# Performance work log

Hardware: AMD Instinct MI355X
Metric: run time of the kernel (lower is better)

## Reference

```python
import jax, jax.numpy as jnp
import numpy as np

N = 50000        # nodes (== input_dim, featureless layer)
E = 400000       # edges in sparse support
HID = 200        # hidden dim hardcoded in GCN
NUM_CLASSES = 10


def setup_inputs() -> dict:
    key = jax.random.key(0)
    k1, k2, k3, k4 = jax.random.split(key, 4)
    return {
        "x": jnp.zeros((N, 1), dtype=jnp.float32),  # unused (featureless layer1)
        "support_rows": jax.random.randint(k1, (E,), 0, N, dtype=jnp.int32),
        "support_cols": jax.random.randint(k2, (E,), 0, N, dtype=jnp.int32),
        "support_vals": jax.random.uniform(k3, (E,), dtype=jnp.float32),
        "W0": jax.random.normal(k4, (N, HID), dtype=jnp.float32),
        "W2": jax.random.normal(jax.random.fold_in(key, 5), (HID, NUM_CLASSES), dtype=jnp.float32),
    }


def reference(x, support_rows, support_cols, support_vals, W0, W2):
    # Layer 1 (featureless): pre_sup = W0; out = A @ W0 via sparse edge list.
    # SpMM as gather + scale + segment-sum:
    gathered = W0[support_cols] * support_vals[:, None]          # [E, HID]
    h = jax.ops.segment_sum(gathered, support_rows, num_segments=N)  # [N, HID]
    h = jax.nn.relu(h)
    # Layer 2 (SimpleGraphConvolution, no act, no bias): h @ W2
    return h @ W2                                                # [N, NUM_CLASSES]
```

## Files before the change

kernel.cpp:

```cpp
#include <hip/hip_runtime.h>

#define N_NODES 50000
#define N_EDGES 400000
#define HID     200
#define NCLS    10
#define SLOTS   40


__device__ __forceinline__ unsigned bf16rn(float f) {
    unsigned u = __float_as_uint(f);
    return (u + 0x7FFFu + ((u >> 16) & 1u)) >> 16;
}
__device__ __forceinline__ float bl(unsigned u) { return __uint_as_float(u << 16); }
__device__ __forceinline__ float bh(unsigned u) { return __uint_as_float(u & 0xFFFF0000u); }

__global__ __launch_bounds__(256) void k_convert(const float4* __restrict__ W04,
                                                 uint4* __restrict__ W0h4,
                                                 int4* __restrict__ cnt4) {
    int i = blockIdx.x * 256 + threadIdx.x;
    if (i < 12504) cnt4[i] = make_int4(0, 0, 0, 0);
    if (i >= (N_NODES * HID) / 8) return;
    float4 f0 = W04[i * 2];
    float4 f1 = W04[i * 2 + 1];
    uint4 o;
    o.x = bf16rn(f0.x) | (bf16rn(f0.y) << 16);
    o.y = bf16rn(f0.z) | (bf16rn(f0.w) << 16);
    o.z = bf16rn(f1.x) | (bf16rn(f1.y) << 16);
    o.w = bf16rn(f1.z) | (bf16rn(f1.w) << 16);
    W0h4[i] = o;
}

__global__ void k_place(const int* __restrict__ rows, const int* __restrict__ cols,
                        const float* __restrict__ vals,
                        int* __restrict__ cnt, unsigned* __restrict__ ev) {
    int e = blockIdx.x * 256 + threadIdx.x;
    if (e >= N_EDGES) return;
    int r = rows[e];
    int pos = atomicAdd(&cnt[r], 1);
    if (pos < SLOTS)
        ev[(size_t)r * SLOTS + pos] = (bf16rn(vals[e]) << 16) | (unsigned)cols[e];
}

__global__ __launch_bounds__(256, 4) void gcn_fused(
        const int*      __restrict__ cnt,
        const unsigned* __restrict__ ev,
        const ushort*   __restrict__ W0h,
        const float*    __restrict__ W2,
        float*          __restrict__ out) {
    __shared__ float w2p[25 * 81 + 7];
    {
        int t = threadIdx.x;
        if (t < HID) {
            float* dst = &w2p[(t >> 3) * 81 + (t & 7) * 10];
            const float* src = &W2[t * NCLS];
            *reinterpret_cast<float4*>(dst)     = *reinterpret_cast<const float4*>(src);
            *reinterpret_cast<float4*>(dst + 4) = *reinterpret_cast<const float4*>(src + 4);
            *reinterpret_cast<float2*>(dst + 8) = *reinterpret_cast<const float2*>(src + 8);
        }
    }
    __syncthreads();

    const int lane = threadIdx.x & 63;
    const int hl   = lane & 31;
    const bool selB = lane >= 32;
    const int lp   = min(hl, 24);
    const int off8 = lp * 8;
    const float* __restrict__ w2l = &w2p[lp * 81];

    const int w  = (blockIdx.x * 256 + threadIdx.x) >> 6;
    const int wu = __builtin_amdgcn_readfirstlane(w);

    const int4 cc = *reinterpret_cast<const int4*>(cnt + 4 * wu);
    const int nA = min(cc.x, SLOTS), nB = min(cc.y, SLOTS);
    const int nC = min(cc.z, SLOTS), nD = min(cc.w, SLOTS);
    const int n0 = selB ? nC : nA;
    const int n1 = selB ? nD : nB;
    const int ntm = (max(max(nA, nB), max(nC, nD)) + 7) >> 3;

    const unsigned* __restrict__ evp = ev + (size_t)(4 * wu) * SLOTS;

    float hk0[8] = {0.f, 0.f, 0.f, 0.f, 0.f, 0.f, 0.f, 0.f};
    float hk1[8] = {0.f, 0.f, 0.f, 0.f, 0.f, 0.f, 0.f, 0.f};

    for (int t = 0; t < ntm; ++t) {
        const int s = t * 8;
        const uint4 a0 = *reinterpret_cast<const uint4*>(evp + s);
        const uint4 a1 = *reinterpret_cast<const uint4*>(evp + s + 4);
        const uint4 b0 = *reinterpret_cast<const uint4*>(evp + SLOTS + s);
        const uint4 b1 = *reinterpret_cast<const uint4*>(evp + SLOTS + s + 4);
        const uint4 c0 = *reinterpret_cast<const uint4*>(evp + 2 * SLOTS + s);
        const uint4 c1 = *reinterpret_cast<const uint4*>(evp + 2 * SLOTS + s + 4);
        const uint4 d0 = *reinterpret_cast<const uint4*>(evp + 3 * SLOTS + s);
        const uint4 d1 = *reinterpret_cast<const uint4*>(evp + 3 * SLOTS + s + 4);

        unsigned u0 = (s + 0 < n0) ? (selB ? c0.x : a0.x) : 0u;
        unsigned u1 = (s + 1 < n0) ? (selB ? c0.y : a0.y) : 0u;
        unsigned u2 = (s + 2 < n0) ? (selB ? c0.z : a0.z) : 0u;
        unsigned u3 = (s + 3 < n0) ? (selB ? c0.w : a0.w) : 0u;
        unsigned u4 = (s + 4 < n0) ? (selB ? c1.x : a1.x) : 0u;
        unsigned u5 = (s + 5 < n0) ? (selB ? c1.y : a1.y) : 0u;
        unsigned u6 = (s + 6 < n0) ? (selB ? c1.z : a1.z) : 0u;
        unsigned u7 = (s + 7 < n0) ? (selB ? c1.w : a1.w) : 0u;
        unsigned v0 = (s + 0 < n1) ? (selB ? d0.x : b0.x) : 0u;
        unsigned v1 = (s + 1 < n1) ? (selB ? d0.y : b0.y) : 0u;
        unsigned v2 = (s + 2 < n1) ? (selB ? d0.z : b0.z) : 0u;
        unsigned v3 = (s + 3 < n1) ? (selB ? d0.w : b0.w) : 0u;
        unsigned v4 = (s + 4 < n1) ? (selB ? d1.x : b1.x) : 0u;
        unsigned v5 = (s + 5 < n1) ? (selB ? d1.y : b1.y) : 0u;
        unsigned v6 = (s + 6 < n1) ? (selB ? d1.z : b1.z) : 0u;
        unsigned v7 = (s + 7 < n1) ? (selB ? d1.w : b1.w) : 0u;

        uint4 gA0 = *reinterpret_cast<const uint4*>(W0h + (size_t)(u0 & 0xFFFFu) * HID + off8);
        uint4 gA1 = *reinterpret_cast<const uint4*>(W0h + (size_t)(u1 & 0xFFFFu) * HID + off8);
        uint4 gA2 = *reinterpret_cast<const uint4*>(W0h + (size_t)(u2 & 0xFFFFu) * HID + off8);
        uint4 gA3 = *reinterpret_cast<const uint4*>(W0h + (size_t)(u3 & 0xFFFFu) * HID + off8);
        uint4 gA4 = *reinterpret_cast<const uint4*>(W0h + (size_t)(u4 & 0xFFFFu) * HID + off8);
        uint4 gA5 = *reinterpret_cast<const uint4*>(W0h + (size_t)(u5 & 0xFFFFu) * HID + off8);
        uint4 gA6 = *reinterpret_cast<const uint4*>(W0h + (size_t)(u6 & 0xFFFFu) * HID + off8);
        uint4 gA7 = *reinterpret_cast<const uint4*>(W0h + (size_t)(u7 & 0xFFFFu) * HID + off8);
        uint4 gB0 = *reinterpret_cast<const uint4*>(W0h + (size_t)(v0 & 0xFFFFu) * HID + off8);
        uint4 gB1 = *reinterpret_cast<const uint4*>(W0h + (size_t)(v1 & 0xFFFFu) * HID + off8);
        uint4 gB2 = *reinterpret_cast<const uint4*>(W0h + (size_t)(v2 & 0xFFFFu) * HID + off8);
        uint4 gB3 = *reinterpret_cast<const uint4*>(W0h + (size_t)(v3 & 0xFFFFu) * HID + off8);
        uint4 gB4 = *reinterpret_cast<const uint4*>(W0h + (size_t)(v4 & 0xFFFFu) * HID + off8);
        uint4 gB5 = *reinterpret_cast<const uint4*>(W0h + (size_t)(v5 & 0xFFFFu) * HID + off8);
        uint4 gB6 = *reinterpret_cast<const uint4*>(W0h + (size_t)(v6 & 0xFFFFu) * HID + off8);
        uint4 gB7 = *reinterpret_cast<const uint4*>(W0h + (size_t)(v7 & 0xFFFFu) * HID + off8);

#define FMA8(H, g, q) {                                                 \
        float vv = bh(q);                                               \
        H[0] += vv * bl((g).x);  H[1] += vv * bh((g).x);                \
        H[2] += vv * bl((g).y);  H[3] += vv * bh((g).y);                \
        H[4] += vv * bl((g).z);  H[5] += vv * bh((g).z);                \
        H[6] += vv * bl((g).w);  H[7] += vv * bh((g).w); }
        FMA8(hk0, gA0, u0); FMA8(hk0, gA1, u1); FMA8(hk0, gA2, u2); FMA8(hk0, gA3, u3);
        FMA8(hk0, gA4, u4); FMA8(hk0, gA5, u5); FMA8(hk0, gA6, u6); FMA8(hk0, gA7, u7);
        FMA8(hk1, gB0, v0); FMA8(hk1, gB1, v1); FMA8(hk1, gB2, v2); FMA8(hk1, gB3, v3);
        FMA8(hk1, gB4, v4); FMA8(hk1, gB5, v5); FMA8(hk1, gB6, v6); FMA8(hk1, gB7, v7);
#undef FMA8
    }

    float acc0[NCLS], acc1[NCLS];
#pragma unroll
    for (int c = 0; c < NCLS; ++c) { acc0[c] = 0.f; acc1[c] = 0.f; }
#pragma unroll
    for (int j = 0; j < 8; ++j) {
        float x0 = fmaxf(hk0[j], 0.f);
        float x1 = fmaxf(hk1[j], 0.f);
#pragma unroll
        for (int c = 0; c < NCLS; ++c) {
            float wv = w2l[j * 10 + c];
            acc0[c] += x0 * wv;
            acc1[c] += x1 * wv;
        }
    }
    const float gate = (hl < 25) ? 1.f : 0.f;
#pragma unroll
    for (int c = 0; c < NCLS; ++c) { acc0[c] *= gate; acc1[c] *= gate; }

#pragma unroll
    for (int c = 0; c < NCLS; ++c) {
#pragma unroll
        for (int off = 16; off >= 1; off >>= 1) {
            acc0[c] += __shfl_xor(acc0[c], off, 32);
            acc1[c] += __shfl_xor(acc1[c], off, 32);
        }
    }

    if (hl == 0) {
        float* o = out + (size_t)(4 * w + (selB ? 2 : 0)) * NCLS;
        *reinterpret_cast<float4*>(o)      = make_float4(acc0[0], acc0[1], acc0[2], acc0[3]);
        *reinterpret_cast<float4*>(o + 4)  = make_float4(acc0[4], acc0[5], acc0[6], acc0[7]);
        *reinterpret_cast<float4*>(o + 8)  = make_float4(acc0[8], acc0[9], acc1[0], acc1[1]);
        *reinterpret_cast<float4*>(o + 12) = make_float4(acc1[2], acc1[3], acc1[4], acc1[5]);
        *reinterpret_cast<float4*>(o + 16) = make_float4(acc1[6], acc1[7], acc1[8], acc1[9]);
    }
}

extern "C" void kernel_launch(void* const* d_in, const int* in_sizes, int n_in,
                              void* d_out, int out_size, void* d_ws, size_t ws_size,
                              hipStream_t stream) {
    const int*   rows = (const int*)  d_in[1];
    const int*   cols = (const int*)  d_in[2];
    const float* vals = (const float*)d_in[3];
    const float* W0   = (const float*)d_in[4];
    const float* W2   = (const float*)d_in[5];
    float*       out  = (float*)d_out;

    char* ws = (char*)d_ws;
    int*      cnt = (int*)     (ws);
    unsigned* ev  = (unsigned*)(ws + 200064);
    ushort*   W0h = (ushort*)  (ws + 8200064);

    int blocksC = ((N_NODES * HID) / 8 + 255) / 256;
    int blocksE = (N_EDGES + 255) / 256;

    k_convert<<<blocksC, 256, 0, stream>>>((const float4*)W0, (uint4*)W0h, (int4*)cnt);
    k_place  <<<blocksE, 256, 0, stream>>>(rows, cols, vals, cnt, ev);

    gcn_fused<<<3125, 256, 0, stream>>>(cnt, ev, W0h, W2, out);
}
```

Baseline: 70.83 us.

## Drop bf16 conversion pass and gather fp32 W0 rows directly

Removes the k_convert kernel that rewrote all of W0 to bf16 each call, leaving a small zeroing kernel for the counters. The edge slot list now stores the full int column and fp32 value as an int2, and the fused kernel gathers fp32 W0 rows as two float4 loads per edge. This removes a full read and write of W0 plus a launch, and restores full precision. In exchange it doubles the bytes per random gather and per slot-list read, and the main loop is split into two half-batches, which may change register use.

```diff
diff --git a/kernel.cpp b/kernel.cpp
--- a/kernel.cpp
+++ b/kernel.cpp
@@ -7,44 +7,28 @@
 #define SLOTS   40
 
 
-__device__ __forceinline__ unsigned bf16rn(float f) {
-    unsigned u = __float_as_uint(f);
-    return (u + 0x7FFFu + ((u >> 16) & 1u)) >> 16;
-}
-__device__ __forceinline__ float bl(unsigned u) { return __uint_as_float(u << 16); }
-__device__ __forceinline__ float bh(unsigned u) { return __uint_as_float(u & 0xFFFF0000u); }
-
-__global__ __launch_bounds__(256) void k_convert(const float4* __restrict__ W04,
-                                                 uint4* __restrict__ W0h4,
-                                                 int4* __restrict__ cnt4) {
+__device__ __forceinline__ float asf(unsigned u) { return __uint_as_float(u); }
+
+__global__ __launch_bounds__(256) void k_zero(int4* __restrict__ cnt4) {
     int i = blockIdx.x * 256 + threadIdx.x;
     if (i < 12504) cnt4[i] = make_int4(0, 0, 0, 0);
-    if (i >= (N_NODES * HID) / 8) return;
-    float4 f0 = W04[i * 2];
-    float4 f1 = W04[i * 2 + 1];
-    uint4 o;
-    o.x = bf16rn(f0.x) | (bf16rn(f0.y) << 16);
-    o.y = bf16rn(f0.z) | (bf16rn(f0.w) << 16);
-    o.z = bf16rn(f1.x) | (bf16rn(f1.y) << 16);
-    o.w = bf16rn(f1.z) | (bf16rn(f1.w) << 16);
-    W0h4[i] = o;
 }
 
 __global__ void k_place(const int* __restrict__ rows, const int* __restrict__ cols,
                         const float* __restrict__ vals,
-                        int* __restrict__ cnt, unsigned* __restrict__ ev) {
+                        int* __restrict__ cnt, int2* __restrict__ ev) {
     int e = blockIdx.x * 256 + threadIdx.x;
     if (e >= N_EDGES) return;
     int r = rows[e];
     int pos = atomicAdd(&cnt[r], 1);
     if (pos < SLOTS)
-        ev[(size_t)r * SLOTS + pos] = (bf16rn(vals[e]) << 16) | (unsigned)cols[e];
+        ev[(size_t)r * SLOTS + pos] = make_int2(cols[e], __float_as_int(vals[e]));
 }
 
 __global__ __launch_bounds__(256, 4) void gcn_fused(
         const int*      __restrict__ cnt,
         const unsigned* __restrict__ ev,
-        const ushort*   __restrict__ W0h,
+        const float*    __restrict__ W0,
         const float*    __restrict__ W2,
         float*          __restrict__ out) {
     __shared__ float w2p[25 * 81 + 7];
@@ -77,68 +61,102 @@
     const int n1 = selB ? nD : nB;
     const int ntm = (max(max(nA, nB), max(nC, nD)) + 7) >> 3;
 
-    const unsigned* __restrict__ evp = ev + (size_t)(4 * wu) * SLOTS;
+    const unsigned* __restrict__ evp = ev + (size_t)(4 * wu) * SLOTS * 2;
 
     float hk0[8] = {0.f, 0.f, 0.f, 0.f, 0.f, 0.f, 0.f, 0.f};
     float hk1[8] = {0.f, 0.f, 0.f, 0.f, 0.f, 0.f, 0.f, 0.f};
 
+#define GLO(c)  (*reinterpret_cast<const float4*>(W0 + (size_t)(c) * HID + off8))
+#define GHI(c)  (*reinterpret_cast<const float4*>(W0 + (size_t)(c) * HID + off8 + 4))
+#define FMA8F(H, gl, gh, vv) {                                          \
+        H[0] += (vv) * (gl).x;  H[1] += (vv) * (gl).y;                  \
+        H[2] += (vv) * (gl).z;  H[3] += (vv) * (gl).w;                  \
+        H[4] += (vv) * (gh).x;  H[5] += (vv) * (gh).y;                  \
+        H[6] += (vv) * (gh).z;  H[7] += (vv) * (gh).w; }
+
     for (int t = 0; t < ntm; ++t) {
-        const int s = t * 8;
-        const uint4 a0 = *reinterpret_cast<const uint4*>(evp + s);
-        const uint4 a1 = *reinterpret_cast<const uint4*>(evp + s + 4);
-        const uint4 b0 = *reinterpret_cast<const uint4*>(evp + SLOTS + s);
-        const uint4 b1 = *reinterpret_cast<const uint4*>(evp + SLOTS + s + 4);
-        const uint4 c0 = *reinterpret_cast<const uint4*>(evp + 2 * SLOTS + s);
-        const uint4 c1 = *reinterpret_cast<const uint4*>(evp + 2 * SLOTS + s + 4);
-        const uint4 d0 = *reinterpret_cast<const uint4*>(evp + 3 * SLOTS + s);
-        const uint4 d1 = *reinterpret_cast<const uint4*>(evp + 3 * SLOTS + s + 4);
-
-        unsigned u0 = (s + 0 < n0) ? (selB ? c0.x : a0.x) : 0u;
-        unsigned u1 = (s + 1 < n0) ? (selB ? c0.y : a0.y) : 0u;
-        unsigned u2 = (s + 2 < n0) ? (selB ? c0.z : a0.z) : 0u;
-        unsigned u3 = (s + 3 < n0) ? (selB ? c0.w : a0.w) : 0u;
-        unsigned u4 = (s + 4 < n0) ? (selB ? c1.x : a1.x) : 0u;
-        unsigned u5 = (s + 5 < n0) ? (selB ? c1.y : a1.y) : 0u;
-        unsigned u6 = (s + 6 < n0) ? (selB ? c1.z : a1.z) : 0u;
-        unsigned u7 = (s + 7 < n0) ? (selB ? c1.w : a1.w) : 0u;
-        unsigned v0 = (s + 0 < n1) ? (selB ? d0.x : b0.x) : 0u;
-        unsigned v1 = (s + 1 < n1) ? (selB ? d0.y : b0.y) : 0u;
-        unsigned v2 = (s + 2 < n1) ? (selB ? d0.z : b0.z) : 0u;
-        unsigned v3 = (s + 3 < n1) ? (selB ? d0.w : b0.w) : 0u;
-        unsigned v4 = (s + 4 < n1) ? (selB ? d1.x : b1.x) : 0u;
-        unsigned v5 = (s + 5 < n1) ? (selB ? d1.y : b1.y) : 0u;
-        unsigned v6 = (s + 6 < n1) ? (selB ? d1.z : b1.z) : 0u;
-        unsigned v7 = (s + 7 < n1) ? (selB ? d1.w : b1.w) : 0u;
-
-        uint4 gA0 = *reinterpret_cast<const uint4*>(W0h + (size_t)(u0 & 0xFFFFu) * HID + off8);
-        uint4 gA1 = *reinterpret_cast<const uint4*>(W0h + (size_t)(u1 & 0xFFFFu) * HID + off8);
-        uint4 gA2 = *reinterpret_cast<const uint4*>(W0h + (size_t)(u2 & 0xFFFFu) * HID + off8);
-        uint4 gA3 = *reinterpret_cast<const uint4*>(W0h + (size_t)(u3 & 0xFFFFu) * HID + off8);
-        uint4 gA4 = *reinterpret_cast<const uint4*>(W0h + (size_t)(u4 & 0xFFFFu) * HID + off8);
-        uint4 gA5 = *reinterpret_cast<const uint4*>(W0h + (size_t)(u5 & 0xFFFFu) * HID + off8);
-        uint4 gA6 = *reinterpret_cast<const uint4*>(W0h + (size_t)(u6 & 0xFFFFu) * HID + off8);
-        uint4 gA7 = *reinterpret_cast<const uint4*>(W0h + (size_t)(u7 & 0xFFFFu) * HID + off8);
-        uint4 gB0 = *reinterpret_cast<const uint4*>(W0h + (size_t)(v0 & 0xFFFFu) * HID + off8);
-        uint4 gB1 = *reinterpret_cast<const uint4*>(W0h + (size_t)(v1 & 0xFFFFu) * HID + off8);
-        uint4 gB2 = *reinterpret_cast<const uint4*>(W0h + (size_t)(v2 & 0xFFFFu) * HID + off8);
-        uint4 gB3 = *reinterpret_cast<const uint4*>(W0h + (size_t)(v3 & 0xFFFFu) * HID + off8);
-        uint4 gB4 = *reinterpret_cast<const uint4*>(W0h + (size_t)(v4 & 0xFFFFu) * HID + off8);
-        uint4 gB5 = *reinterpret_cast<const uint4*>(W0h + (size_t)(v5 & 0xFFFFu) * HID + off8);
-        uint4 gB6 = *reinterpret_cast<const uint4*>(W0h + (size_t)(v6 & 0xFFFFu) * HID + off8);
-        uint4 gB7 = *reinterpret_cast<const uint4*>(W0h + (size_t)(v7 & 0xFFFFu) * HID + off8);
-
-#define FMA8(H, g, q) {                                                 \
-        float vv = bh(q);                                               \
-        H[0] += vv * bl((g).x);  H[1] += vv * bh((g).x);                \
-        H[2] += vv * bl((g).y);  H[3] += vv * bh((g).y);                \
-        H[4] += vv * bl((g).z);  H[5] += vv * bh((g).z);                \
-        H[6] += vv * bl((g).w);  H[7] += vv * bh((g).w); }
-        FMA8(hk0, gA0, u0); FMA8(hk0, gA1, u1); FMA8(hk0, gA2, u2); FMA8(hk0, gA3, u3);
-        FMA8(hk0, gA4, u4); FMA8(hk0, gA5, u5); FMA8(hk0, gA6, u6); FMA8(hk0, gA7, u7);
-        FMA8(hk1, gB0, v0); FMA8(hk1, gB1, v1); FMA8(hk1, gB2, v2); FMA8(hk1, gB3, v3);
-        FMA8(hk1, gB4, v4); FMA8(hk1, gB5, v5); FMA8(hk1, gB6, v6); FMA8(hk1, gB7, v7);
-#undef FMA8
-    }
+        const int s  = t * 8;
+        const int sb = s * 2;
+        const uint4 qa0 = *reinterpret_cast<const uint4*>(evp + sb);
+        const uint4 qa1 = *reinterpret_cast<const uint4*>(evp + sb + 4);
+        const uint4 qa2 = *reinterpret_cast<const uint4*>(evp + sb + 8);
+        const uint4 qa3 = *reinterpret_cast<const uint4*>(evp + sb + 12);
+        const uint4 qb0 = *reinterpret_cast<const uint4*>(evp + 2*SLOTS + sb);
+        const uint4 qb1 = *reinterpret_cast<const uint4*>(evp + 2*SLOTS + sb + 4);
+        const uint4 qb2 = *reinterpret_cast<const uint4*>(evp + 2*SLOTS + sb + 8);
+        const uint4 qb3 = *reinterpret_cast<const uint4*>(evp + 2*SLOTS + sb + 12);
+        const uint4 qc0 = *reinterpret_cast<const uint4*>(evp + 4*SLOTS + sb);
+        const uint4 qc1 = *reinterpret_cast<const uint4*>(evp + 4*SLOTS + sb + 4);
+        const uint4 qc2 = *reinterpret_cast<const uint4*>(evp + 4*SLOTS + sb + 8);
+        const uint4 qc3 = *reinterpret_cast<const uint4*>(evp + 4*SLOTS + sb + 12);
+        const uint4 qd0 = *reinterpret_cast<const uint4*>(evp + 6*SLOTS + sb);
+        const uint4 qd1 = *reinterpret_cast<const uint4*>(evp + 6*SLOTS + sb + 4);
+        const uint4 qd2 = *reinterpret_cast<const uint4*>(evp + 6*SLOTS + sb + 8);
+        const uint4 qd3 = *reinterpret_cast<const uint4*>(evp + 6*SLOTS + sb + 12);
+
+        unsigned f0c = (s+0 < n0) ? (selB ? qc0.x : qa0.x) : 0u;
+        float    f0v = (s+0 < n0) ? asf(selB ? qc0.y : qa0.y) : 0.f;
+        unsigned f1c = (s+1 < n0) ? (selB ? qc0.z : qa0.z) : 0u;
+        float    f1v = (s+1 < n0) ? asf(selB ? qc0.w : qa0.w) : 0.f;
+        unsigned f2c = (s+2 < n0) ? (selB ? qc1.x : qa1.x) : 0u;
+        float    f2v = (s+2 < n0) ? asf(selB ? qc1.y : qa1.y) : 0.f;
+        unsigned f3c = (s+3 < n0) ? (selB ? qc1.z : qa1.z) : 0u;
+        float    f3v = (s+3 < n0) ? asf(selB ? qc1.w : qa1.w) : 0.f;
+        unsigned g0c = (s+0 < n1) ? (selB ? qd0.x : qb0.x) : 0u;
+        float    g0v = (s+0 < n1) ? asf(selB ? qd0.y : qb0.y) : 0.f;
+        unsigned g1c = (s+1 < n1) ? (selB ? qd0.z : qb0.z) : 0u;
+        float    g1v = (s+1 < n1) ? asf(selB ? qd0.w : qb0.w) : 0.f;
+        unsigned g2c = (s+2 < n1) ? (selB ? qd1.x : qb1.x) : 0u;
+        float    g2v = (s+2 < n1) ? asf(selB ? qd1.y : qb1.y) : 0.f;
+        unsigned g3c = (s+3 < n1) ? (selB ? qd1.z : qb1.z) : 0u;
+        float    g3v = (s+3 < n1) ? asf(selB ? qd1.w : qb1.w) : 0.f;
+
+        float4 a0l = GLO(f0c), a0h = GHI(f0c);
+        float4 a1l = GLO(f1c), a1h = GHI(f1c);
+        float4 a2l = GLO(f2c), a2h = GHI(f2c);
+        float4 a3l = GLO(f3c), a3h = GHI(f3c);
+        float4 b0l = GLO(g0c), b0h = GHI(g0c);
+        float4 b1l = GLO(g1c), b1h = GHI(g1c);
+        float4 b2l = GLO(g2c), b2h = GHI(g2c);
+        float4 b3l = GLO(g3c), b3h = GHI(g3c);
+        FMA8F(hk0, a0l, a0h, f0v); FMA8F(hk0, a1l, a1h, f1v);
+        FMA8F(hk0, a2l, a2h, f2v); FMA8F(hk0, a3l, a3h, f3v);
+        FMA8F(hk1, b0l, b0h, g0v); FMA8F(hk1, b1l, b1h, g1v);
+        FMA8F(hk1, b2l, b2h, g2v); FMA8F(hk1, b3l, b3h, g3v);
+
+        unsigned f4c = (s+4 < n0) ? (selB ? qc2.x : qa2.x) : 0u;
+        float    f4v = (s+4 < n0) ? asf(selB ? qc2.y : qa2.y) : 0.f;
+        unsigned f5c = (s+5 < n0) ? (selB ? qc2.z : qa2.z) : 0u;
+        float    f5v = (s+5 < n0) ? asf(selB ? qc2.w : qa2.w) : 0.f;
+        unsigned f6c = (s+6 < n0) ? (selB ? qc3.x : qa3.x) : 0u;
+        float    f6v = (s+6 < n0) ? asf(selB ? qc3.y : qa3.y) : 0.f;
+        unsigned f7c = (s+7 < n0) ? (selB ? qc3.z : qa3.z) : 0u;
+        float    f7v = (s+7 < n0) ? asf(selB ? qc3.w : qa3.w) : 0.f;
+        unsigned g4c = (s+4 < n1) ? (selB ? qd2.x : qb2.x) : 0u;
+        float    g4v = (s+4 < n1) ? asf(selB ? qd2.y : qb2.y) : 0.f;
+        unsigned g5c = (s+5 < n1) ? (selB ? qd2.z : qb2.z) : 0u;
+        float    g5v = (s+5 < n1) ? asf(selB ? qd2.w : qb2.w) : 0.f;
+        unsigned g6c = (s+6 < n1) ? (selB ? qd3.x : qb3.x) : 0u;
+        float    g6v = (s+6 < n1) ? asf(selB ? qd3.y : qb3.y) : 0.f;
+        unsigned g7c = (s+7 < n1) ? (selB ? qd3.z : qb3.z) : 0u;
+        float    g7v = (s+7 < n1) ? asf(selB ? qd3.w : qb3.w) : 0.f;
+
+        float4 c0l = GLO(f4c), c0h = GHI(f4c);
+        float4 c1l = GLO(f5c), c1h = GHI(f5c);
+        float4 c2l = GLO(f6c), c2h = GHI(f6c);
+        float4 c3l = GLO(f7c), c3h = GHI(f7c);
+        float4 d0l = GLO(g4c), d0h = GHI(g4c);
+        float4 d1l = GLO(g5c), d1h = GHI(g5c);
+        float4 d2l = GLO(g6c), d2h = GHI(g6c);
+        float4 d3l = GLO(g7c), d3h = GHI(g7c);
+        FMA8F(hk0, c0l, c0h, f4v); FMA8F(hk0, c1l, c1h, f5v);
+        FMA8F(hk0, c2l, c2h, f6v); FMA8F(hk0, c3l, c3h, f7v);
+        FMA8F(hk1, d0l, d0h, g4v); FMA8F(hk1, d1l, d1h, g5v);
+        FMA8F(hk1, d2l, d2h, g6v); FMA8F(hk1, d3l, d3h, g7v);
+    }
+#undef GLO
+#undef GHI
+#undef FMA8F
 
     float acc0[NCLS], acc1[NCLS];
 #pragma unroll
@@ -188,15 +206,13 @@
     float*       out  = (float*)d_out;
 
     char* ws = (char*)d_ws;
-    int*      cnt = (int*)     (ws);
-    unsigned* ev  = (unsigned*)(ws + 200064);
-    ushort*   W0h = (ushort*)  (ws + 8200064);
-
-    int blocksC = ((N_NODES * HID) / 8 + 255) / 256;
+    int*  cnt = (int*) (ws);
+    int2* ev  = (int2*)(ws + 200064);
+
     int blocksE = (N_EDGES + 255) / 256;
 
-    k_convert<<<blocksC, 256, 0, stream>>>((const float4*)W0, (uint4*)W0h, (int4*)cnt);
-    k_place  <<<blocksE, 256, 0, stream>>>(rows, cols, vals, cnt, ev);
-
-    gcn_fused<<<3125, 256, 0, stream>>>(cnt, ev, W0h, W2, out);
-}
+    k_zero <<<49, 256, 0, stream>>>((int4*)cnt);
+    k_place<<<blocksE, 256, 0, stream>>>(rows, cols, vals, cnt, ev);
+
+    gcn_fused<<<3125, 256, 0, stream>>>(cnt, (const unsigned*)ev, W0, W2, out);
+}
```

Measured after the change: 94.07 us. 32.8% more time.
